# Kernel tuning notes

Hardware: AMD Instinct MI355X
Metric: run time of the kernel (lower is better)

## Reference

```python
import jax, jax.numpy as jnp
import numpy as np

# mcorrlcorr hyperparameters (closed over as constants; int args to the op)
S = (1, 2)   # stride (sx, sy)
D = (1, 1)   # dilation (dx, dy)
P = (0, 2)   # padding (px, py)
U = (1, 1)   # upsample / input dilation (ux, uy)
R = (0, 0)   # extra output size (rx, ry)


def _out_sizes(nfx, nfy, ngx, ngy):
    sx, sy = S; dx, dy = D; px, py = P; ux, uy = U; rx, ry = R
    # mcorr_valid_size along x, lcorr_valid_size along y (from source)
    nhx = max((ngx + ux - 1) * (px + 1) // (nfx + dx - 1) - sx + 1, 0) + rx
    nhy = max((uy * (ngy - 1) - dy * (nfy - 1) + py) // sy + 1, 0) + ry
    return nhx, nhy


def setup_inputs() -> dict:
    key = jax.random.key(0)
    k1, k2, k3 = jax.random.split(key, 3)
    input = jax.random.normal(k1, (16, 32, 128, 384), dtype=jnp.float32)
    weight = jax.random.normal(k2, (64, 32, 4, 8), dtype=jnp.float32) * 0.05
    bias = jax.random.normal(k3, (64,), dtype=jnp.float32) * 0.05
    return {"input": input, "weight": weight, "bias": bias}


def _mcorrlcorr(input, weight, bias):
    batch, c_in, ngx, ngy = input.shape
    c_out, _, nfx, nfy = weight.shape
    sx, sy = S; dx, dy = D; px, py = P; ux, uy = U
    nhx, nhy = _out_sizes(nfx, nfy, ngx, ngy)
    px1 = px + 1

    # --- multiplicative (Mellin) correlation along x ---
    # gx = (hx+sx)*(fx+dx)/(px+1) - ux  when divisible and in [0, ngx)
    hx = jnp.arange(nhx)
    fxi = jnp.arange(nfx)
    num_x = (hx[:, None] + sx) * (fxi[None, :] + dx)          # [nhx, nfx]
    gx = num_x // px1 - ux
    vx = (num_x % px1 == 0) & (gx >= 0) & (gx < ngx)
    gxc = jnp.clip(gx, 0, ngx - 1)
    # gather along x: G1[b, c, hx, fx, gy_full]
    G1 = input[:, :, gxc, :] * vx.astype(input.dtype)[None, None, :, :, None]

    # contract channels and fx, keep fy separate: U[b, o, hx, fy, ngy]
    Ufy = jnp.einsum('bcxfg,ocfy->boxyg', G1, weight)

    # --- linear correlation along y ---
    # gy = (sy*hy - py + dy*fy)/uy  when divisible and in [0, ngy)
    hy = jnp.arange(nhy)
    fyi = jnp.arange(nfy)
    num_y = sy * hy[:, None] - py + dy * fyi[None, :]          # [nhy, nfy]
    gy = num_y // uy
    vy = (num_y % uy == 0) & (gy >= 0) & (gy < ngy)
    gyc = jnp.clip(gy, 0, ngy - 1)

    def gather_fy(Uf, gyf, vyf):
        # Uf: [b, o, nhx, ngy]; gyf, vyf: [nhy]
        return Uf[..., gyf] * vyf.astype(Uf.dtype)

    # vmap over fy axis (axis 3 of Ufy, axis 1 of gyc/vy) -> [nfy, b, o, nhx, nhy]
    per_fy = jax.vmap(gather_fy, in_axes=(3, 1, 1), out_axes=0)(Ufy, gyc, vy)
    h = per_fy.sum(0) + bias[None, :, None, None]
    return h


def reference(input, weight, bias):
    return _mcorrlcorr(input, weight, bias)
```

## Files before the change

### kernel.cpp

```cpp
#include <hip/hip_runtime.h>
#include <hip/hip_bf16.h>


#define Bb   16
#define NGX  128
#define NGY  384
#define Oo   64
#define NHX  32
#define NHY  190

#define RSX  398
#define XBUF (16 * RSX)
#define ATIL 4096

typedef short bf16x8 __attribute__((ext_vector_type(8)));
typedef float f32x4  __attribute__((ext_vector_type(4)));

__device__ __forceinline__ unsigned short f2bf(float f) {
  __hip_bfloat16 h = __float2bfloat16(f);
  return __builtin_bit_cast(unsigned short, h);
}

__global__ void wprep_kernel(const float* __restrict__ w, unsigned short* __restrict__ wl) {
  int idx = blockIdx.x * 256 + threadIdx.x;
  if (idx >= Oo * 1024) return;
  int ac = idx >> 12;
  int g  = ac >> 3, t = ac & 7;
  int o  = (idx >> 6) & 63;
  int p  = idx & 63;
  wl[idx] = f2bf(w[o * 1024 + 512 * g + 64 * t + (p ^ (8 * (o & 7)))]);
}

__global__ __launch_bounds__(512, 4)
void mcorr_mfma_kernel(const float* __restrict__ in, const unsigned short* __restrict__ wl,
                       const float* __restrict__ bias, float* __restrict__ out) {
  const int tid  = threadIdx.x;
  const int l    = tid & 63;
  const int wv   = tid >> 6;
  const int kg   = wv >> 2;
  const int whq  = wv & 3;
  const int lo16 = l & 15, gq = l >> 4;

  int lid = blockIdx.x + NHX * blockIdx.y;
  int swz = (lid & 7) * 64 + (lid >> 3);
  const int hx = swz & 31;
  const int b  = swz >> 5;

  __shared__ unsigned short smem[2 * 2 * ATIL + 2 * XBUF];
  unsigned short* As_ = smem;
  unsigned short* xs_ = smem + 4 * ATIL;

  f32x4 acc[4][3];
  #pragma unroll
  for (int i = 0; i < 4; ++i)
    #pragma unroll
    for (int j = 0; j < 3; ++j) acc[i][j] = (f32x4){0.f, 0.f, 0.f, 0.f};

  for (int i = tid; i < 2 * 16 * 14; i += 512) {
    int j   = i % 14;
    int row = (i / 14) % 16;
    int buf = i / (14 * 16);
    int p   = (j < 2) ? j : (384 + j);
    xs_[buf * XBUF + row * RSX + p] = 0;
  }

  const int r_st  = tid >> 5;
  const int j0    = tid & 31;
  const int fx_st = r_st & 3;
  const int cb_st = 16 * (r_st >> 3) + ((r_st >> 2) & 1);
  const int gx_st = (hx + 1) * (fx_st + 1) - 1;
  const float* xbase = in + (((size_t)b * 32 + cb_st) * NGX + gx_st) * NGY;
  const size_t cstep = (size_t)2 * NGX * NGY;

  float4 xv[3];

#define AISSUE(T, BI)                                                                \
  do {                                                                               \
    _Pragma("unroll") for (int g_ = 0; g_ < 2; ++g_)                                 \
      __builtin_amdgcn_global_load_lds(                                              \
          (const __attribute__((address_space(1))) void*)                            \
              (wl + (size_t)(g_ * 8 + (T)) * ATIL + tid * 8),                        \
          (__attribute__((address_space(3))) void*)                                  \
              (As_ + (BI) * 2 * ATIL + g_ * ATIL + tid * 8),                         \
          16, 0, 0);                                                                 \
  } while (0)

#define XLOAD(T)                                                         \
  do {                                                                   \
    const float* xb_ = xbase + (size_t)(T) * cstep;                      \
    _Pragma("unroll") for (int s_ = 0; s_ < 3; ++s_)                     \
      xv[s_] = *(const float4*)(xb_ + 4 * j0 + 128 * s_);                \
  } while (0)

#define XCOMMIT(T)                                                       \
  do {                                                                   \
    unsigned short* row_ = xs_ + ((T) & 1) * XBUF + r_st * RSX;          \
    _Pragma("unroll") for (int s_ = 0; s_ < 3; ++s_) {                   \
      int p_ = 2 + 4 * j0 + 128 * s_;                                    \
      ushort2 h0_; h0_.x = f2bf(xv[s_].x); h0_.y = f2bf(xv[s_].y);       \
      ushort2 h1_; h1_.x = f2bf(xv[s_].z); h1_.y = f2bf(xv[s_].w);       \
      *(ushort2*)&row_[p_]     = h0_;                                    \
      *(ushort2*)&row_[p_ + 2] = h1_;                                    \
    }                                                                    \
  } while (0)

#define COMPUTE(T)                                                                   \
  do {                                                                               \
    const unsigned short* Ab_ = As_ + ((T) & 1) * 2 * ATIL + kg * ATIL;              \
    const unsigned* Xb_ = (const unsigned*)(xs_ + ((T) & 1) * XBUF);                 \
    _Pragma("unroll") for (int cs_ = 0; cs_ < 2; ++cs_) {                            \
      const int q_ = (32 * cs_ + 8 * gq) ^ (8 * (lo16 & 7));                         \
      bf16x8 a_[4];                                                                  \
      _Pragma("unroll") for (int mt_ = 0; mt_ < 4; ++mt_)                            \
        a_[mt_] = *(const bf16x8*)&Ab_[(16 * mt_ + lo16) * 64 + q_];                 \
      const int r_ = kg * 8 + 4 * cs_ + gq;                                          \
      _Pragma("unroll") for (int tt_ = 0; tt_ < 3; ++tt_) {                          \
        int hy_ = 48 * whq + 16 * tt_ + lo16;                                        \
        const unsigned* xp_ = &Xb_[r_ * 199 + hy_];                                  \
        union { unsigned u[4]; bf16x8 v; } bb_;                                      \
        bb_.u[0] = xp_[0]; bb_.u[1] = xp_[1];                                        \
        bb_.u[2] = xp_[2]; bb_.u[3] = xp_[3];                                        \
        _Pragma("unroll") for (int mt_ = 0; mt_ < 4; ++mt_)                          \
          acc[mt_][tt_] = __builtin_amdgcn_mfma_f32_16x16x32_bf16(                   \
              a_[mt_], bb_.v, acc[mt_][tt_], 0, 0, 0);                               \
      }                                                                              \
    }                                                                                \
  } while (0)

  AISSUE(0, 0);
  XLOAD(0);
  XCOMMIT(0);
  __syncthreads();

  #pragma unroll
  for (int t = 0; t < 8; ++t) {
    if (t < 7) {
      AISSUE(t + 1, (t & 1) ^ 1);
      XLOAD(t + 1);
    }
    COMPUTE(t);
    if (t < 7) {
      XCOMMIT(t + 1);
      __syncthreads();
    }
  }

  __syncthreads();
  float* red = (float*)smem;
  if (kg == 1) {
    #pragma unroll
    for (int mt = 0; mt < 4; ++mt)
      #pragma unroll
      for (int tt = 0; tt < 3; ++tt)
        *(f32x4*)&red[whq * 3072 + (mt * 3 + tt) * 256 + l * 4] = acc[mt][tt];
  }
  __syncthreads();
  if (kg == 0) {
    #pragma unroll
    for (int mt = 0; mt < 4; ++mt) {
      #pragma unroll
      for (int tt = 0; tt < 3; ++tt) {
        f32x4 v = *(const f32x4*)&red[whq * 3072 + (mt * 3 + tt) * 256 + l * 4];
        acc[mt][tt] += v;
      }
    }
    #pragma unroll
    for (int mt = 0; mt < 4; ++mt) {
      #pragma unroll
      for (int reg = 0; reg < 4; ++reg) {
        int o = 16 * mt + 4 * gq + reg;
        float bv = bias[o];
        #pragma unroll
        for (int tt = 0; tt < 3; ++tt) {
          int hy = 48 * whq + 16 * tt + lo16;
          if (hy < NHY)
            out[(((size_t)b * Oo + o) * NHX + hx) * NHY + hy] = acc[mt][tt][reg] + bv;
        }
      }
    }
  }
}

extern "C" void kernel_launch(void* const* d_in, const int* in_sizes, int n_in,
                              void* d_out, int out_size, void* d_ws, size_t ws_size,
                              hipStream_t stream) {
  const float* in   = (const float*)d_in[0];
  const float* w    = (const float*)d_in[1];
  const float* bias = (const float*)d_in[2];
  float* out = (float*)d_out;
  unsigned short* wl = (unsigned short*)d_ws;

  wprep_kernel<<<(Oo * 1024 + 255) / 256, 256, 0, stream>>>(w, wl);

  dim3 grid(NHX, Bb);
  mcorr_mfma_kernel<<<grid, 512, 0, stream>>>(in, wl, bias, out);
}
```

Baseline: 34.04 us.

## Split output channels across wave groups and read weights directly from global

The work split changes from two wave groups each covering half the channel range (K) to two wave groups each covering half the output channels over the full K range. This removes the shared-memory cross-group reduction and its extra barriers. Weight tiles are no longer staged in LDS through global_load_lds; each wave reads bf16 fragments straight from a re-laid-out global weight buffer, relying on L1/L2 caching. Input staging now double-buffers register loads two steps ahead, widens LDS stores to 4-element vectors and realigns rows with a 4-element head. Barriers are replaced by an lgkmcnt wait plus s_barrier, and the trade is more global weight traffic per block in exchange for less LDS use and no reduction.

```diff
diff --git a/kernel.cpp b/kernel.cpp
--- a/kernel.cpp
+++ b/kernel.cpp
@@ -9,12 +9,13 @@
 #define NHX  32
 #define NHY  190
 
-#define RSX  398
+#define HEAD 4
+#define RSX  400
 #define XBUF (16 * RSX)
-#define ATIL 4096
 
 typedef short bf16x8 __attribute__((ext_vector_type(8)));
 typedef float f32x4  __attribute__((ext_vector_type(4)));
+typedef unsigned short u16x4 __attribute__((ext_vector_type(4)));
 
 __device__ __forceinline__ unsigned short f2bf(float f) {
   __hip_bfloat16 h = __float2bfloat16(f);
@@ -24,11 +25,10 @@
 __global__ void wprep_kernel(const float* __restrict__ w, unsigned short* __restrict__ wl) {
   int idx = blockIdx.x * 256 + threadIdx.x;
   if (idx >= Oo * 1024) return;
-  int ac = idx >> 12;
-  int g  = ac >> 3, t = ac & 7;
-  int o  = (idx >> 6) & 63;
-  int p  = idx & 63;
-  wl[idx] = f2bf(w[o * 1024 + 512 * g + 64 * t + (p ^ (8 * (o & 7)))]);
+  int k8 = idx >> 9;
+  int o  = (idx >> 3) & 63;
+  int j  = idx & 7;
+  wl[idx] = f2bf(w[o * 1024 + k8 * 8 + j]);
 }
 
 __global__ __launch_bounds__(512, 4)
@@ -37,7 +37,7 @@
   const int tid  = threadIdx.x;
   const int l    = tid & 63;
   const int wv   = tid >> 6;
-  const int kg   = wv >> 2;
+  const int wo   = wv >> 2;
   const int whq  = wv & 3;
   const int lo16 = l & 15, gq = l >> 4;
 
@@ -46,136 +46,95 @@
   const int hx = swz & 31;
   const int b  = swz >> 5;
 
-  __shared__ unsigned short smem[2 * 2 * ATIL + 2 * XBUF];
-  unsigned short* As_ = smem;
-  unsigned short* xs_ = smem + 4 * ATIL;
+  __shared__ __align__(16) unsigned short xs_[2 * XBUF];
 
-  f32x4 acc[4][3];
+  f32x4 acc[2][3];
   #pragma unroll
-  for (int i = 0; i < 4; ++i)
+  for (int i = 0; i < 2; ++i)
     #pragma unroll
     for (int j = 0; j < 3; ++j) acc[i][j] = (f32x4){0.f, 0.f, 0.f, 0.f};
 
-  for (int i = tid; i < 2 * 16 * 14; i += 512) {
-    int j   = i % 14;
-    int row = (i / 14) % 16;
-    int buf = i / (14 * 16);
-    int p   = (j < 2) ? j : (384 + j);
-    xs_[buf * XBUF + row * RSX + p] = 0;
+  {
+    int bu = tid >> 8, row = (tid >> 4) & 15, j = tid & 15;
+    xs_[bu * XBUF + row * RSX + (j < HEAD ? j : 384 + j)] = 0;
   }
 
   const int r_st  = tid >> 5;
   const int j0    = tid & 31;
   const int fx_st = r_st & 3;
-  const int cb_st = 16 * (r_st >> 3) + ((r_st >> 2) & 1);
+  const int c_st  = r_st >> 2;
   const int gx_st = (hx + 1) * (fx_st + 1) - 1;
-  const float* xbase = in + (((size_t)b * 32 + cb_st) * NGX + gx_st) * NGY;
-  const size_t cstep = (size_t)2 * NGX * NGY;
+  const float* xbase = in + (((size_t)b * 32 + c_st) * NGX + gx_st) * NGY;
+  const size_t cstep = (size_t)4 * NGX * NGY;
 
-  float4 xv[3];
+  float4 xv[2][3];
 
-#define AISSUE(T, BI)                                                                \
-  do {                                                                               \
-    _Pragma("unroll") for (int g_ = 0; g_ < 2; ++g_)                                 \
-      __builtin_amdgcn_global_load_lds(                                              \
-          (const __attribute__((address_space(1))) void*)                            \
-              (wl + (size_t)(g_ * 8 + (T)) * ATIL + tid * 8),                        \
-          (__attribute__((address_space(3))) void*)                                  \
-              (As_ + (BI) * 2 * ATIL + g_ * ATIL + tid * 8),                         \
-          16, 0, 0);                                                                 \
+#define XLOAD(T) do {                                                    \
+    const float* xb_ = xbase + (size_t)(T) * cstep;                      \
+    _Pragma("unroll") for (int s_ = 0; s_ < 3; ++s_)                     \
+      xv[(T) & 1][s_] = *(const float4*)(xb_ + 4 * j0 + 128 * s_);       \
   } while (0)
 
-#define XLOAD(T)                                                         \
-  do {                                                                   \
-    const float* xb_ = xbase + (size_t)(T) * cstep;                      \
-    _Pragma("unroll") for (int s_ = 0; s_ < 3; ++s_)                     \
-      xv[s_] = *(const float4*)(xb_ + 4 * j0 + 128 * s_);                \
-  } while (0)
-
-#define XCOMMIT(T)                                                       \
-  do {                                                                   \
+#define XCOMMIT(T) do {                                                  \
     unsigned short* row_ = xs_ + ((T) & 1) * XBUF + r_st * RSX;          \
     _Pragma("unroll") for (int s_ = 0; s_ < 3; ++s_) {                   \
-      int p_ = 2 + 4 * j0 + 128 * s_;                                    \
-      ushort2 h0_; h0_.x = f2bf(xv[s_].x); h0_.y = f2bf(xv[s_].y);       \
-      ushort2 h1_; h1_.x = f2bf(xv[s_].z); h1_.y = f2bf(xv[s_].w);       \
-      *(ushort2*)&row_[p_]     = h0_;                                    \
-      *(ushort2*)&row_[p_ + 2] = h1_;                                    \
+      u16x4 h_;                                                          \
+      h_[0] = f2bf(xv[(T) & 1][s_].x); h_[1] = f2bf(xv[(T) & 1][s_].y);  \
+      h_[2] = f2bf(xv[(T) & 1][s_].z); h_[3] = f2bf(xv[(T) & 1][s_].w);  \
+      *(u16x4*)&row_[HEAD + 4 * j0 + 128 * s_] = h_;                     \
     }                                                                    \
   } while (0)
 
-#define COMPUTE(T)                                                                   \
-  do {                                                                               \
-    const unsigned short* Ab_ = As_ + ((T) & 1) * 2 * ATIL + kg * ATIL;              \
+#define BAR() do {                                                       \
+    asm volatile("s_waitcnt lgkmcnt(0)" ::: "memory");                   \
+    __builtin_amdgcn_s_barrier();                                        \
+  } while (0)
+
+#define COMPUTE(T) do {                                                              \
     const unsigned* Xb_ = (const unsigned*)(xs_ + ((T) & 1) * XBUF);                 \
-    _Pragma("unroll") for (int cs_ = 0; cs_ < 2; ++cs_) {                            \
-      const int q_ = (32 * cs_ + 8 * gq) ^ (8 * (lo16 & 7));                         \
-      bf16x8 a_[4];                                                                  \
-      _Pragma("unroll") for (int mt_ = 0; mt_ < 4; ++mt_)                            \
-        a_[mt_] = *(const bf16x8*)&Ab_[(16 * mt_ + lo16) * 64 + q_];                 \
-      const int r_ = kg * 8 + 4 * cs_ + gq;                                          \
+    _Pragma("unroll") for (int cs_ = 0; cs_ < 4; ++cs_) {                            \
+      const unsigned short* ap_ =                                                    \
+          wl + ((4 * (T) + cs_) * 4 + gq) * 512 + (32 * wo + lo16) * 8;              \
+      bf16x8 a0_ = *(const bf16x8*)ap_;                                              \
+      bf16x8 a1_ = *(const bf16x8*)(ap_ + 128);                           \
+      const int r_ = cs_ * 4 + gq;                                                   \
       _Pragma("unroll") for (int tt_ = 0; tt_ < 3; ++tt_) {                          \
         int hy_ = 48 * whq + 16 * tt_ + lo16;                                        \
-        const unsigned* xp_ = &Xb_[r_ * 199 + hy_];                                  \
+        const unsigned* xp_ = &Xb_[r_ * 200 + 1 + hy_];                              \
         union { unsigned u[4]; bf16x8 v; } bb_;                                      \
         bb_.u[0] = xp_[0]; bb_.u[1] = xp_[1];                                        \
         bb_.u[2] = xp_[2]; bb_.u[3] = xp_[3];                                        \
-        _Pragma("unroll") for (int mt_ = 0; mt_ < 4; ++mt_)                          \
-          acc[mt_][tt_] = __builtin_amdgcn_mfma_f32_16x16x32_bf16(                   \
-              a_[mt_], bb_.v, acc[mt_][tt_], 0, 0, 0);                               \
+        acc[0][tt_] = __builtin_amdgcn_mfma_f32_16x16x32_bf16(                       \
+            a0_, bb_.v, acc[0][tt_], 0, 0, 0);                                       \
+        acc[1][tt_] = __builtin_amdgcn_mfma_f32_16x16x32_bf16(                       \
+            a1_, bb_.v, acc[1][tt_], 0, 0, 0);                                       \
       }                                                                              \
     }                                                                                \
   } while (0)
 
-  AISSUE(0, 0);
   XLOAD(0);
+  XLOAD(1);
   XCOMMIT(0);
-  __syncthreads();
+  BAR();
 
   #pragma unroll
   for (int t = 0; t < 8; ++t) {
-    if (t < 7) {
-      AISSUE(t + 1, (t & 1) ^ 1);
-      XLOAD(t + 1);
-    }
+    if (t < 6) XLOAD(t + 2);
     COMPUTE(t);
-    if (t < 7) {
-      XCOMMIT(t + 1);
-      __syncthreads();
-    }
+    if (t < 7) { XCOMMIT(t + 1); BAR(); }
   }
 
-  __syncthreads();
-  float* red = (float*)smem;
-  if (kg == 1) {
+  #pragma unroll
+  for (int mt = 0; mt < 2; ++mt) {
     #pragma unroll
-    for (int mt = 0; mt < 4; ++mt)
-      #pragma unroll
-      for (int tt = 0; tt < 3; ++tt)
-        *(f32x4*)&red[whq * 3072 + (mt * 3 + tt) * 256 + l * 4] = acc[mt][tt];
-  }
-  __syncthreads();
-  if (kg == 0) {
-    #pragma unroll
-    for (int mt = 0; mt < 4; ++mt) {
+    for (int reg = 0; reg < 4; ++reg) {
+      int o = 32 * wo + 16 * mt + 4 * gq + reg;
+      float bv = bias[o];
       #pragma unroll
       for (int tt = 0; tt < 3; ++tt) {
-        f32x4 v = *(const f32x4*)&red[whq * 3072 + (mt * 3 + tt) * 256 + l * 4];
-        acc[mt][tt] += v;
-      }
-    }
-    #pragma unroll
-    for (int mt = 0; mt < 4; ++mt) {
-      #pragma unroll
-      for (int reg = 0; reg < 4; ++reg) {
-        int o = 16 * mt + 4 * gq + reg;
-        float bv = bias[o];
-        #pragma unroll
-        for (int tt = 0; tt < 3; ++tt) {
-          int hy = 48 * whq + 16 * tt + lo16;
-          if (hy < NHY)
-            out[(((size_t)b * Oo + o) * NHX + hx) * NHY + hy] = acc[mt][tt][reg] + bv;
-        }
+        int hy = 48 * whq + 16 * tt + lo16;
+        if (hy < NHY)
+          out[(((size_t)b * Oo + o) * NHX + hx) * NHY + hy] = acc[mt][tt][reg] + bv;
       }
     }
   }
```

Measured after the change: 32.72 us. -3.9%, faster.
